# Kernel optimization log

Hardware: AMD Instinct MI355X
Metric: run time of the kernel (lower is better)

## Reference

```python
import jax, jax.numpy as jnp
import numpy as np
import math

BS, QL, KL = 2, 2048, 2048
H, D = 16, 64          # n_heads, cell_dim
QS = KS = VS = 1024    # query/key/value feature sizes
HD = H * D


def setup_inputs() -> dict:
    key = jax.random.key(0)
    ks = jax.random.split(key, 12)
    s_in = 1.0 / math.sqrt(QS)
    s_hd = 1.0 / math.sqrt(HD)
    return {
        "query": jax.random.normal(ks[0], (BS, QL, QS), jnp.float32),
        "key": jax.random.normal(ks[1], (BS, KL, KS), jnp.float32),
        "value": jax.random.normal(ks[2], (BS, KL, VS), jnp.float32),
        # nn.Linear weights stored as [in, out] for x @ W + b
        "Wq_w": jax.random.normal(ks[3], (QS, HD), jnp.float32) * s_in,
        "Wq_b": jax.random.normal(ks[4], (HD,), jnp.float32) * s_in,
        "Wk_w": jax.random.normal(ks[5], (KS, HD), jnp.float32) * s_in,
        "Wk_b": jax.random.normal(ks[6], (HD,), jnp.float32) * s_in,
        "Wv_w": jax.random.normal(ks[7], (VS, HD), jnp.float32) * s_in,
        "Wv_b": jax.random.normal(ks[8], (HD,), jnp.float32) * s_in,
        "Wo_w": jax.random.normal(ks[9], (HD, HD), jnp.float32) * s_hd,
        "Wo_b": jax.random.normal(ks[10], (HD,), jnp.float32) * s_hd,
    }


def reference(query, key, value, Wq_w, Wq_b, Wk_w, Wk_b, Wv_w, Wv_b, Wo_w, Wo_b):
    bs, ql, _ = query.shape
    kl = key.shape[1]
    # project and split heads; torch .chunk along dim 2 == head-major reshape
    q = (query @ Wq_w + Wq_b).reshape(bs, ql, H, D).transpose(0, 2, 1, 3)  # bhqd
    k = (key @ Wk_w + Wk_b).reshape(bs, kl, H, D).transpose(0, 2, 1, 3)    # bhkd
    v = (value @ Wv_w + Wv_b).reshape(bs, kl, H, D).transpose(0, 2, 1, 3)  # bhkd
    scores = jnp.einsum("bhqd,bhkd->bhqk", q, k) / jnp.sqrt(jnp.float32(D))
    # log_softmax(...).exp() == softmax (use_mask=False path)
    w = jax.nn.softmax(scores, axis=-1)
    heads = jnp.einsum("bhqk,bhkd->bhqd", w, v)
    out = heads.transpose(0, 2, 1, 3).reshape(bs, ql, HD)  # concat heads on dim 2
    return out @ Wo_w + Wo_b
```

## Files before the change

### kernel.cpp

```cpp
#include <hip/hip_runtime.h>

#define BSZ 2
#define SEQ 2048
#define NH 16
#define DHD 64
#define HDIM 1024
#define FS 1024
#define MR (BSZ*SEQ)
#define L2E 1.4426950408889634f

typedef __bf16 bf16x8 __attribute__((ext_vector_type(8)));
typedef __bf16 bf16x2t __attribute__((ext_vector_type(2)));
typedef float f32x4 __attribute__((ext_vector_type(4)));
typedef float f32x16 __attribute__((ext_vector_type(16)));
typedef unsigned short u16;
typedef unsigned int u32;
typedef u32 u32x4 __attribute__((ext_vector_type(4)));

__device__ __forceinline__ u16 f2bf(float f) {
  u32 x = __float_as_uint(f);
  return (u16)((x + 0x7fffu + ((x >> 16) & 1u)) >> 16);
}

__device__ __forceinline__ u32 pack2bf(float a, float b) {
  bf16x2t t = {(__bf16)a, (__bf16)b};
  return __builtin_bit_cast(u32, t);
}

__device__ __forceinline__ void gload16(const void* g, void* l) {
  __builtin_amdgcn_global_load_lds(
      (const __attribute__((address_space(1))) u32*)g,
      (__attribute__((address_space(3))) u32*)l, 16, 0, 0);
}

__global__ __launch_bounds__(256) void transw4_k(
    const float* __restrict__ W0, const float* __restrict__ W1,
    const float* __restrict__ W2, const float* __restrict__ W3,
    u16* __restrict__ WTbase) {
  __shared__ float t[32][33];
  const int z = blockIdx.z;
  const float* W = z == 0 ? W0 : z == 1 ? W1 : z == 2 ? W2 : W3;
  u16* WT = WTbase + (size_t)z * FS * HDIM;
  const int tx = threadIdx.x, ty = threadIdx.y;
  const int c0 = blockIdx.x * 32, r0 = blockIdx.y * 32;
#pragma unroll
  for (int i = 0; i < 4; i++)
    t[ty + 8 * i][tx] = W[(size_t)(r0 + ty + 8 * i) * FS + c0 + tx];
  __syncthreads();
#pragma unroll
  for (int i = 0; i < 4; i++)
    WT[(size_t)(c0 + ty + 8 * i) * FS + r0 + tx] = f2bf(t[tx][ty + 8 * i]);
}

__global__ __launch_bounds__(256, 2) void gemmQKV_k(
    const float* __restrict__ qf32, const float* __restrict__ kf32,
    const float* __restrict__ vf32, const u16* __restrict__ WTbase,
    const float* __restrict__ bq, const float* __restrict__ bk,
    const float* __restrict__ bv, u16* __restrict__ QKbase,
    u16* __restrict__ VpT) {
  __shared__ u16 aL[128 * 64];
  __shared__ u16 bL[2][128 * 64];
  const int grp = blockIdx.y;
  const float* Af = grp == 0 ? qf32 : grp == 1 ? kf32 : vf32;
  const u16* BT = WTbase + (size_t)grp * FS * HDIM;
  const float* bias = grp == 0 ? bq : grp == 1 ? bk : bv;
  const int bx = blockIdx.x;
  const int m0 = (4 * (bx & 7) + (bx >> 6)) << 7;
  const int n0 = ((bx >> 3) & 7) << 7;
  const int tid = threadIdx.x, w = tid >> 6, lane = tid & 63;
  const int wr = ((w >> 1) << 6), wc = ((w & 1) << 6);
  const int li = lane & 15, g = lane >> 4;

  f32x4 acc[4][4];
#pragma unroll
  for (int i = 0; i < 4; i++)
#pragma unroll
    for (int j = 0; j < 4; j++) acc[i][j] = (f32x4){0.f, 0.f, 0.f, 0.f};

  const float* asrc[4];
  const u16* bsrc[4];
  int ldoff[4];
#pragma unroll
  for (int j = 0; j < 4; j++) {
    const int c = w * 4 + j;
    const int r = c * 8 + (lane >> 3);
    const int sc = (lane & 7) ^ (r & 7);
    asrc[j] = Af + (size_t)(m0 + r) * FS + sc * 8;
    bsrc[j] = BT + (size_t)(n0 + r) * FS + sc * 8;
    ldoff[j] = c * 1024;
  }

  float4 ar0[4], ar1[4];
#pragma unroll
  for (int j = 0; j < 4; j++) gload16(bsrc[j], (char*)bL[0] + ldoff[j]);
#pragma unroll
  for (int j = 0; j < 4; j++) {
    ar0[j] = *(const float4*)(asrc[j]);
    ar1[j] = *(const float4*)(asrc[j] + 4);
  }

  for (int kt = 0; kt < 16; kt++) {
    const int cur = kt & 1;
#pragma unroll
    for (int j = 0; j < 4; j++) {
      u32x4 pk;
      pk[0] = pack2bf(ar0[j].x, ar0[j].y);
      pk[1] = pack2bf(ar0[j].z, ar0[j].w);
      pk[2] = pack2bf(ar1[j].x, ar1[j].y);
      pk[3] = pack2bf(ar1[j].z, ar1[j].w);
      *(u32x4*)((char*)aL + ldoff[j] + lane * 16) = pk;
    }
    __syncthreads();
    if (kt + 1 < 16) {
      const int ko = (kt + 1) * 64;
#pragma unroll
      for (int j = 0; j < 4; j++)
        gload16(bsrc[j] + ko, (char*)bL[cur ^ 1] + ldoff[j]);
#pragma unroll
      for (int j = 0; j < 4; j++) {
        ar0[j] = *(const float4*)(asrc[j] + ko);
        ar1[j] = *(const float4*)(asrc[j] + ko + 4);
      }
    }
    bf16x8 af[2][4], bfr[2][4];
#pragma unroll
    for (int ks = 0; ks < 2; ks++) {
#pragma unroll
      for (int mf = 0; mf < 4; mf++) {
        const int r = wr + mf * 16 + li;
        const int sl = (g + 4 * ks) ^ (r & 7);
        af[ks][mf] = *(const bf16x8*)((const char*)aL + r * 128 + sl * 16);
      }
#pragma unroll
      for (int nf = 0; nf < 4; nf++) {
        const int r = wc + nf * 16 + li;
        const int sl = (g + 4 * ks) ^ (r & 7);
        bfr[ks][nf] = *(const bf16x8*)((const char*)bL[cur] + r * 128 + sl * 16);
      }
    }
#pragma unroll
    for (int ks = 0; ks < 2; ks++)
#pragma unroll
      for (int mf = 0; mf < 4; mf++)
#pragma unroll
        for (int nf = 0; nf < 4; nf++)
          acc[mf][nf] = __builtin_amdgcn_mfma_f32_16x16x32_bf16(
              af[ks][mf], bfr[ks][nf], acc[mf][nf], 0, 0, 0);
    __syncthreads();
  }

  if (grp < 2) {
    const float osc = grp == 0 ? 0.125f * L2E : 1.0f;
    u16* C = QKbase + (size_t)grp * MR * HDIM;
#pragma unroll
    for (int mf = 0; mf < 4; mf++)
#pragma unroll
      for (int nf = 0; nf < 4; nf++) {
        const int n = n0 + wc + nf * 16 + li;
        const float bvl = bias[n];
#pragma unroll
        for (int r4 = 0; r4 < 4; r4++) {
          const int m = m0 + wr + mf * 16 + g * 4 + r4;
          C[(size_t)m * HDIM + n] = f2bf((acc[mf][nf][r4] + bvl) * osc);
        }
      }
  } else {
#pragma unroll
    for (int mf = 0; mf < 4; mf++)
#pragma unroll
      for (int nf = 0; nf < 4; nf++) {
        const int n = n0 + wc + nf * 16 + li;
        const float bvl = bias[n];
        const int m = m0 + wr + mf * 16 + g * 4;
        const int bb = m >> 11, kv = m & 2047;
        ushort4 o;
        o.x = f2bf(acc[mf][nf][0] + bvl);
        o.y = f2bf(acc[mf][nf][1] + bvl);
        o.z = f2bf(acc[mf][nf][2] + bvl);
        o.w = f2bf(acc[mf][nf][3] + bvl);
        *(ushort4*)(VpT +
                    ((size_t)(bb * NH + (n >> 6)) * DHD + (n & 63)) * SEQ + kv) = o;
      }
  }
}

__global__ __launch_bounds__(256, 2) void gemm_out_k(
    const u16* __restrict__ A, const u16* __restrict__ BT,
    const float* __restrict__ bias, float* __restrict__ C) {
  __shared__ u16 aL[128 * 64];
  __shared__ u16 bL[128 * 64];
  const int bx = blockIdx.x;
  const int m0 = (4 * (bx & 7) + (bx >> 6)) << 7;
  const int n0 = ((bx >> 3) & 7) << 7;
  const int tid = threadIdx.x, w = tid >> 6, lane = tid & 63;
  const int wr = ((w >> 1) << 6), wc = ((w & 1) << 6);
  const int li = lane & 15, g = lane >> 4;

  f32x4 acc[4][4];
#pragma unroll
  for (int i = 0; i < 4; i++)
#pragma unroll
    for (int j = 0; j < 4; j++) acc[i][j] = (f32x4){0.f, 0.f, 0.f, 0.f};

  for (int k0 = 0; k0 < HDIM; k0 += 64) {
#pragma unroll
    for (int j = 0; j < 4; j++) {
      const int c = w * 4 + j;
      const int r = c * 8 + (lane >> 3);
      const int sc = (lane & 7) ^ (r & 7);
      gload16(A + (size_t)(m0 + r) * HDIM + k0 + sc * 8, (char*)aL + c * 1024);
      gload16(BT + (size_t)(n0 + r) * HDIM + k0 + sc * 8, (char*)bL + c * 1024);
    }
    __syncthreads();
    bf16x8 af[2][4], bfr[2][4];
#pragma unroll
    for (int ks = 0; ks < 2; ks++) {
#pragma unroll
      for (int mf = 0; mf < 4; mf++) {
        const int r = wr + mf * 16 + li;
        const int sl = (g + 4 * ks) ^ (r & 7);
        af[ks][mf] = *(const bf16x8*)((const char*)aL + r * 128 + sl * 16);
      }
#pragma unroll
      for (int nf = 0; nf < 4; nf++) {
        const int r = wc + nf * 16 + li;
        const int sl = (g + 4 * ks) ^ (r & 7);
        bfr[ks][nf] = *(const bf16x8*)((const char*)bL + r * 128 + sl * 16);
      }
    }
#pragma unroll
    for (int ks = 0; ks < 2; ks++)
#pragma unroll
      for (int mf = 0; mf < 4; mf++)
#pragma unroll
        for (int nf = 0; nf < 4; nf++)
          acc[mf][nf] = __builtin_amdgcn_mfma_f32_16x16x32_bf16(
              af[ks][mf], bfr[ks][nf], acc[mf][nf], 0, 0, 0);
    __syncthreads();
  }

#pragma unroll
  for (int mf = 0; mf < 4; mf++)
#pragma unroll
    for (int nf = 0; nf < 4; nf++) {
      const int n = n0 + wc + nf * 16 + li;
      const float bvl = bias[n];
#pragma unroll
      for (int r4 = 0; r4 < 4; r4++) {
        const int m = m0 + wr + mf * 16 + g * 4 + r4;
        C[(size_t)m * HDIM + n] = acc[mf][nf][r4] + bvl;
      }
    }
}

__global__ __launch_bounds__(512, 1) void attn_k(
    const u16* __restrict__ Qp, const u16* __restrict__ Kp,
    const u16* __restrict__ VpT, u16* __restrict__ Hd) {
  __shared__ u16 kbuf[4][64 * 64];
  __shared__ u16 vbuf[4][64 * 64];

  const int bid = blockIdx.x;
  const int swz = (bid & 7) * 64 + (bid >> 3);
  const int qb = swz & 15;
  const int h = (swz >> 4) & 15;
  const int b = swz >> 8;
  const int tid = threadIdx.x, w = tid >> 6, lane = tid & 63;
  const int sel = w >> 2, g3 = w & 3;
  const int q32 = lane & 31, hi = lane >> 5;
  const int q0 = qb << 7;
  const size_t qbase = (size_t)(b * SEQ + q0) * HDIM + (size_t)h * DHD;
  const size_t kbase = (size_t)(b * SEQ) * HDIM + (size_t)h * DHD;
  const size_t vtbase = (size_t)(b * NH + h) * DHD * SEQ;

  const int rr = lane >> 3;
  const int sc8 = ((lane & 7) ^ rr) * 8;
  const int fkey = (q32 & 7) << 4;

#pragma unroll
  for (int j = 0; j < 2; j++) {
    const int c = w * 2 + j;
    const int r = c * 8 + rr;
    gload16(Qp + qbase + (size_t)r * HDIM + sc8, (char*)kbuf + c * 1024);
  }
  __syncthreads();
  bf16x8 qf[4];
  {
    const char* qbp = (const char*)kbuf + (g3 * 32 + q32) * 128;
#pragma unroll
    for (int ds = 0; ds < 4; ds++)
      qf[ds] = *(const bf16x8*)(qbp + ((32 * ds + 16 * hi) ^ fkey));
  }
  __syncthreads();

  float mrun = -1e30f, lrun = 0.f;
  f32x16 o0, o1;
#pragma unroll
  for (int i = 0; i < 16; i++) { o0[i] = 0.f; o1[i] = 0.f; }

  const int c0j = g3 * 2;
  const int r0r = c0j * 8 + rr;
  const u16* kp0 = Kp + kbase + (size_t)(r0r + sel * 64) * HDIM + sc8;
  const u16* kp1 = kp0 + (size_t)8 * HDIM;
  const u16* vp0 = VpT + vtbase + (size_t)r0r * SEQ + sel * 64 + sc8;
  const u16* vp1 = vp0 + (size_t)8 * SEQ;
  const int ldk0 = c0j * 1024, ldk1 = (c0j + 1) * 1024;

  auto stage2 = [&](int buf) {
    gload16(kp0, (char*)kbuf[buf] + ldk0);
    gload16(kp1, (char*)kbuf[buf] + ldk1);
    gload16(vp0, (char*)vbuf[buf] + ldk0);
    gload16(vp1, (char*)vbuf[buf] + ldk1);
    kp0 += (size_t)128 * HDIM;
    kp1 += (size_t)128 * HDIM;
    vp0 += 128;
    vp1 += 128;
  };

  stage2(sel);

#pragma unroll 1
  for (int p = 0; p < SEQ / 128; p++) {
    __syncthreads();
    if (p + 1 < SEQ / 128) stage2(sel + 2 * ((p + 1) & 1));
    const char* kl = (const char*)kbuf[sel + 2 * (p & 1)];
    const char* vl = (const char*)vbuf[sel + 2 * (p & 1)];

    f32x16 s0, s1;
#pragma unroll
    for (int i = 0; i < 16; i++) { s0[i] = 0.f; s1[i] = 0.f; }
#pragma unroll
    for (int ds = 0; ds < 4; ds++) {
      const int off = (32 * ds + 16 * hi) ^ fkey;
      const bf16x8 ka = *(const bf16x8*)(kl + q32 * 128 + off);
      const bf16x8 kb2 = *(const bf16x8*)(kl + (32 + q32) * 128 + off);
      s0 = __builtin_amdgcn_mfma_f32_32x32x16_bf16(ka, qf[ds], s0, 0, 0, 0);
      s1 = __builtin_amdgcn_mfma_f32_32x32x16_bf16(kb2, qf[ds], s1, 0, 0, 0);
    }

    float mt[16];
#pragma unroll
    for (int i = 0; i < 16; i++) mt[i] = fmaxf(s0[i], s1[i]);
#pragma unroll
    for (int i = 0; i < 8; i++) mt[i] = fmaxf(mt[i], mt[i + 8]);
#pragma unroll
    for (int i = 0; i < 4; i++) mt[i] = fmaxf(mt[i], mt[i + 4]);
    float mx = fmaxf(fmaxf(mt[0], mt[1]), fmaxf(mt[2], mt[3]));
    mx = fmaxf(mx, __shfl_xor(mx, 32));
    if (!__all(mx <= mrun + 8.0f)) {
      const float mnew = fmaxf(mrun, mx);
      const float scl = __builtin_amdgcn_exp2f(mrun - mnew);
      mrun = mnew;
      lrun *= scl;
#pragma unroll
      for (int i = 0; i < 16; i++) { o0[i] *= scl; o1[i] *= scl; }
    }
    float p0[16], p1[16];
#pragma unroll
    for (int i = 0; i < 16; i++) {
      p0[i] = __builtin_amdgcn_exp2f(s0[i] - mrun);
      p1[i] = __builtin_amdgcn_exp2f(s1[i] - mrun);
    }
    float st[16];
#pragma unroll
    for (int i = 0; i < 16; i++) st[i] = p0[i] + p1[i];
#pragma unroll
    for (int i = 0; i < 8; i++) st[i] += st[i + 8];
#pragma unroll
    for (int i = 0; i < 4; i++) st[i] += st[i + 4];
    float rs = (st[0] + st[1]) + (st[2] + st[3]);
    rs += __shfl_xor(rs, 32);
    lrun += rs;

#pragma unroll
    for (int kvs = 0; kvs < 4; kvs++) {
      const float* ps = (kvs < 2) ? p0 : p1;
      const int rb = (kvs & 1) * 8;
      u32 w01 = pack2bf(ps[rb + 0], ps[rb + 1]);
      u32 w23 = pack2bf(ps[rb + 2], ps[rb + 3]);
      u32 w45 = pack2bf(ps[rb + 4], ps[rb + 5]);
      u32 w67 = pack2bf(ps[rb + 6], ps[rb + 7]);
      asm("v_permlane32_swap_b32 %0, %1" : "+v"(w01), "+v"(w45));
      asm("v_permlane32_swap_b32 %0, %1" : "+v"(w23), "+v"(w67));
      u32x4 uw = {w01, w23, w45, w67};
      const bf16x8 pf = __builtin_bit_cast(bf16x8, uw);
      const int off = (32 * kvs + 16 * hi) ^ fkey;
      const bf16x8 va = *(const bf16x8*)(vl + q32 * 128 + off);
      const bf16x8 vb2 = *(const bf16x8*)(vl + (32 + q32) * 128 + off);
      o0 = __builtin_amdgcn_mfma_f32_32x32x16_bf16(va, pf, o0, 0, 0, 0);
      o1 = __builtin_amdgcn_mfma_f32_32x32x16_bf16(vb2, pf, o1, 0, 0, 0);
    }
  }

  __syncthreads();
  char* mbase = (char*)kbuf + (g3 * 64 + lane) * 144;
  if (sel == 1) {
#pragma unroll
    for (int i = 0; i < 4; i++) {
      *(f32x4*)(mbase + i * 16) =
          (f32x4){o0[4 * i], o0[4 * i + 1], o0[4 * i + 2], o0[4 * i + 3]};
      *(f32x4*)(mbase + 64 + i * 16) =
          (f32x4){o1[4 * i], o1[4 * i + 1], o1[4 * i + 2], o1[4 * i + 3]};
    }
    *(float*)(mbase + 128) = mrun;
    *(float*)(mbase + 132) = lrun;
  }
  __syncthreads();
  if (sel == 0) {
    const float m2 = *(const float*)(mbase + 128);
    const float l2 = *(const float*)(mbase + 132);
    const float ms = fmaxf(mrun, m2);
    const float f1 = __builtin_amdgcn_exp2f(mrun - ms);
    const float f2 = __builtin_amdgcn_exp2f(m2 - ms);
    const float inv = 1.f / (lrun * f1 + l2 * f2);
    const int q = q0 + g3 * 32 + q32;
    u16* orow = Hd + (size_t)(b * SEQ + q) * HDIM + (size_t)h * DHD;
#pragma unroll
    for (int rg = 0; rg < 4; rg++) {
      const f32x4 a2 = *(const f32x4*)(mbase + rg * 16);
      const f32x4 b2 = *(const f32x4*)(mbase + 64 + rg * 16);
      ushort4 ov;
      ov.x = f2bf((o0[4 * rg + 0] * f1 + a2[0] * f2) * inv);
      ov.y = f2bf((o0[4 * rg + 1] * f1 + a2[1] * f2) * inv);
      ov.z = f2bf((o0[4 * rg + 2] * f1 + a2[2] * f2) * inv);
      ov.w = f2bf((o0[4 * rg + 3] * f1 + a2[3] * f2) * inv);
      *(ushort4*)(orow + 8 * rg + 4 * hi) = ov;
      ushort4 ow;
      ow.x = f2bf((o1[4 * rg + 0] * f1 + b2[0] * f2) * inv);
      ow.y = f2bf((o1[4 * rg + 1] * f1 + b2[1] * f2) * inv);
      ow.z = f2bf((o1[4 * rg + 2] * f1 + b2[2] * f2) * inv);
      ow.w = f2bf((o1[4 * rg + 3] * f1 + b2[3] * f2) * inv);
      *(ushort4*)(orow + 32 + 8 * rg + 4 * hi) = ow;
    }
  }
}

extern "C" void kernel_launch(void* const* d_in, const int* in_sizes, int n_in,
                              void* d_out, int out_size, void* d_ws, size_t ws_size,
                              hipStream_t stream) {
  (void)in_sizes; (void)n_in; (void)out_size; (void)ws_size;
  const float* q_in = (const float*)d_in[0];
  const float* k_in = (const float*)d_in[1];
  const float* v_in = (const float*)d_in[2];
  const float* Wq_w = (const float*)d_in[3];
  const float* Wq_b = (const float*)d_in[4];
  const float* Wk_w = (const float*)d_in[5];
  const float* Wk_b = (const float*)d_in[6];
  const float* Wv_w = (const float*)d_in[7];
  const float* Wv_b = (const float*)d_in[8];
  const float* Wo_w = (const float*)d_in[9];
  const float* Wo_b = (const float*)d_in[10];

  char* ws = (char*)d_ws;
  size_t off = 0;
  auto alloc = [&](size_t n) {
    char* p = ws + off;
    off += (n + 255) & ~(size_t)255;
    return p;
  };
  u16* wT = (u16*)alloc((size_t)4 * FS * HDIM * 2);
  u16* QK = (u16*)alloc((size_t)2 * MR * HDIM * 2);
  u16* VpT = (u16*)alloc((size_t)MR * HDIM * 2);
  u16* Hdp = (u16*)alloc((size_t)MR * HDIM * 2);

  transw4_k<<<dim3(FS / 32, FS / 32, 4), dim3(32, 8), 0, stream>>>(
      Wq_w, Wk_w, Wv_w, Wo_w, wT);

  gemmQKV_k<<<dim3(256, 3), 256, 0, stream>>>(q_in, k_in, v_in, wT, Wq_b,
                                              Wk_b, Wv_b, QK, VpT);

  attn_k<<<BSZ * NH * (SEQ / 128), 512, 0, stream>>>(
      QK, QK + (size_t)MR * HDIM, VpT, Hdp);

  gemm_out_k<<<256, 256, 0, stream>>>(Hdp, wT + (size_t)3 * FS * HDIM, Wo_b,
                                      (float*)d_out);
}
```

Baseline: 113.2 us.

## Double-buffer output GEMM loads and halve N tile to double block count

The output projection GEMM now uses two LDS buffers so the next K tile's global loads are issued while MFMAs run on the current tile, with one barrier per iteration instead of two. The N tile shrinks from 128 to 64, doubling the grid to 512 blocks for better CU fill on the 4096x1024 output. The block index swizzle is adjusted to the new grid shape. In exchange, A is reloaded by twice as many blocks and per-block arithmetic intensity drops.

```diff
diff --git a/kernel.cpp b/kernel.cpp
--- a/kernel.cpp
+++ b/kernel.cpp
@@ -187,45 +187,71 @@
 __global__ __launch_bounds__(256, 2) void gemm_out_k(
     const u16* __restrict__ A, const u16* __restrict__ BT,
     const float* __restrict__ bias, float* __restrict__ C) {
-  __shared__ u16 aL[128 * 64];
-  __shared__ u16 bL[128 * 64];
+  __shared__ u16 aL[2][128 * 64];
+  __shared__ u16 bL[2][64 * 64];
   const int bx = blockIdx.x;
-  const int m0 = (4 * (bx & 7) + (bx >> 6)) << 7;
-  const int n0 = ((bx >> 3) & 7) << 7;
+  const int m0 = ((bx & 7) * 4 + (bx >> 7)) << 7;
+  const int n0 = ((bx >> 3) & 15) << 6;
   const int tid = threadIdx.x, w = tid >> 6, lane = tid & 63;
-  const int wr = ((w >> 1) << 6), wc = ((w & 1) << 6);
+  const int wr = ((w >> 1) << 6), wc = ((w & 1) << 5);
   const int li = lane & 15, g = lane >> 4;
 
-  f32x4 acc[4][4];
+  f32x4 acc[4][2];
 #pragma unroll
   for (int i = 0; i < 4; i++)
 #pragma unroll
-    for (int j = 0; j < 4; j++) acc[i][j] = (f32x4){0.f, 0.f, 0.f, 0.f};
-
-  for (int k0 = 0; k0 < HDIM; k0 += 64) {
-#pragma unroll
-    for (int j = 0; j < 4; j++) {
-      const int c = w * 4 + j;
-      const int r = c * 8 + (lane >> 3);
-      const int sc = (lane & 7) ^ (r & 7);
-      gload16(A + (size_t)(m0 + r) * HDIM + k0 + sc * 8, (char*)aL + c * 1024);
-      gload16(BT + (size_t)(n0 + r) * HDIM + k0 + sc * 8, (char*)bL + c * 1024);
-    }
+    for (int j = 0; j < 2; j++) acc[i][j] = (f32x4){0.f, 0.f, 0.f, 0.f};
+
+  const u16* asrc[4];
+  const u16* bsrc[2];
+  int aoff[4], boff[2];
+#pragma unroll
+  for (int j = 0; j < 4; j++) {
+    const int c = w * 4 + j;
+    const int r = c * 8 + (lane >> 3);
+    const int sc = (lane & 7) ^ (r & 7);
+    asrc[j] = A + (size_t)(m0 + r) * HDIM + sc * 8;
+    aoff[j] = c * 1024;
+  }
+#pragma unroll
+  for (int j = 0; j < 2; j++) {
+    const int c = w * 2 + j;
+    const int r = c * 8 + (lane >> 3);
+    const int sc = (lane & 7) ^ (r & 7);
+    bsrc[j] = BT + (size_t)(n0 + r) * HDIM + sc * 8;
+    boff[j] = c * 1024;
+  }
+
+  auto stage = [&](int kt, int buf) {
+    const int ko = kt * 64;
+#pragma unroll
+    for (int j = 0; j < 4; j++)
+      gload16(asrc[j] + ko, (char*)aL[buf] + aoff[j]);
+#pragma unroll
+    for (int j = 0; j < 2; j++)
+      gload16(bsrc[j] + ko, (char*)bL[buf] + boff[j]);
+  };
+
+  stage(0, 0);
+
+  for (int kt = 0; kt < 16; kt++) {
+    const int cur = kt & 1;
     __syncthreads();
-    bf16x8 af[2][4], bfr[2][4];
+    if (kt + 1 < 16) stage(kt + 1, cur ^ 1);
+    bf16x8 af[2][4], bfr[2][2];
 #pragma unroll
     for (int ks = 0; ks < 2; ks++) {
 #pragma unroll
       for (int mf = 0; mf < 4; mf++) {
         const int r = wr + mf * 16 + li;
         const int sl = (g + 4 * ks) ^ (r & 7);
-        af[ks][mf] = *(const bf16x8*)((const char*)aL + r * 128 + sl * 16);
-      }
-#pragma unroll
-      for (int nf = 0; nf < 4; nf++) {
+        af[ks][mf] = *(const bf16x8*)((const char*)aL[cur] + r * 128 + sl * 16);
+      }
+#pragma unroll
+      for (int nf = 0; nf < 2; nf++) {
         const int r = wc + nf * 16 + li;
         const int sl = (g + 4 * ks) ^ (r & 7);
-        bfr[ks][nf] = *(const bf16x8*)((const char*)bL + r * 128 + sl * 16);
+        bfr[ks][nf] = *(const bf16x8*)((const char*)bL[cur] + r * 128 + sl * 16);
       }
     }
 #pragma unroll
@@ -233,16 +259,15 @@
 #pragma unroll
       for (int mf = 0; mf < 4; mf++)
 #pragma unroll
-        for (int nf = 0; nf < 4; nf++)
+        for (int nf = 0; nf < 2; nf++)
           acc[mf][nf] = __builtin_amdgcn_mfma_f32_16x16x32_bf16(
               af[ks][mf], bfr[ks][nf], acc[mf][nf], 0, 0, 0);
-    __syncthreads();
   }
 
 #pragma unroll
   for (int mf = 0; mf < 4; mf++)
 #pragma unroll
-    for (int nf = 0; nf < 4; nf++) {
+    for (int nf = 0; nf < 2; nf++) {
       const int n = n0 + wc + nf * 16 + li;
       const float bvl = bias[n];
 #pragma unroll
@@ -471,6 +496,6 @@
   attn_k<<<BSZ * NH * (SEQ / 128), 512, 0, stream>>>(
       QK, QK + (size_t)MR * HDIM, VpT, Hdp);
 
-  gemm_out_k<<<256, 256, 0, stream>>>(Hdp, wT + (size_t)3 * FS * HDIM, Wo_b,
+  gemm_out_k<<<512, 256, 0, stream>>>(Hdp, wT + (size_t)3 * FS * HDIM, Wo_b,
                                       (float*)d_out);
 }
```

After: 112.1 us (median of 4 runs). Within noise of the previous version (-0.9%).
